# Performance work log

Measured on AMD Instinct MI355X. Metric: run time of the kernel, lower is better.

Reference implementation:

```python
import jax, jax.numpy as jnp
import numpy as np

D_MODEL = 2048
N_HEADS = 16
HEAD_DIM = D_MODEL // N_HEADS
D_FF = 4 * D_MODEL


def setup_inputs() -> dict:
    key = jax.random.key(0)
    ks = jax.random.split(key, 12)
    s = 1.0 / np.sqrt(D_MODEL)
    sf = 1.0 / np.sqrt(D_FF)
    return {
        "x": jax.random.normal(ks[0], (2, 2048, D_MODEL), dtype=jnp.float32),
        "wq": jax.random.uniform(ks[1], (D_MODEL, D_MODEL), jnp.float32, -s, s),
        "wk": jax.random.uniform(ks[2], (D_MODEL, D_MODEL), jnp.float32, -s, s),
        "wv": jax.random.uniform(ks[3], (D_MODEL, D_MODEL), jnp.float32, -s, s),
        "wo": jax.random.uniform(ks[4], (D_MODEL, D_MODEL), jnp.float32, -s, s),
        "w1": jax.random.uniform(ks[5], (D_MODEL, D_FF), jnp.float32, -s, s),
        "b1": jax.random.uniform(ks[6], (D_FF,), jnp.float32, -s, s),
        "w2": jax.random.uniform(ks[7], (D_FF, D_MODEL), jnp.float32, -sf, sf),
        "b2": jax.random.uniform(ks[8], (D_MODEL,), jnp.float32, -sf, sf),
        "g1": jnp.ones((D_MODEL,), jnp.float32),
        "be1": jnp.zeros((D_MODEL,), jnp.float32),
        "g2": jnp.ones((D_MODEL,), jnp.float32),
        "be2": jnp.zeros((D_MODEL,), jnp.float32),
    }


def _layernorm(x, g, b, eps=1e-5):
    mu = jnp.mean(x, axis=-1, keepdims=True)
    var = jnp.mean(jnp.square(x - mu), axis=-1, keepdims=True)
    return (x - mu) * jax.lax.rsqrt(var + eps) * g + b


def reference(x, wq, wk, wv, wo, w1, b1, w2, b2, g1, be1, g2, be2):
    B, S, D = x.shape
    residual = x
    h = _layernorm(x, g1, be1)
    # [B,S,D] -> [B,H,S,hd]
    q = (h @ wq).reshape(B, S, N_HEADS, HEAD_DIM).transpose(0, 2, 1, 3)
    k = (h @ wk).reshape(B, S, N_HEADS, HEAD_DIM).transpose(0, 2, 1, 3)
    v = (h @ wv).reshape(B, S, N_HEADS, HEAD_DIM).transpose(0, 2, 1, 3)
    scores = jnp.einsum("bhqd,bhkd->bhqk", q, k) / np.sqrt(HEAD_DIM).astype(np.float32)
    attn = jax.nn.softmax(scores, axis=-1)
    out = jnp.einsum("bhqk,bhkd->bhqd", attn, v)
    out = out.transpose(0, 2, 1, 3).reshape(B, S, D) @ wo
    x = residual + out
    residual = x
    h = _layernorm(x, g2, be2)
    h = jax.nn.gelu(h @ w1 + b1, approximate=False) @ w2 + b2
    return residual + h
```

## Files before the change

### kernel.cpp

```cpp
#include <hip/hip_runtime.h>
#include <cstdint>
#include <cstddef>

#define DM   2048
#define NH   16
#define HD   128
#define DFF  8192
#define SEQ  2048
#define NB   2
#define NTOK (NB * SEQ)

using bf16x8 = __attribute__((ext_vector_type(8))) __bf16;
using f32x4  = __attribute__((ext_vector_type(4))) float;

__device__ __forceinline__ unsigned short f2bf(float f) {
  unsigned int u = __float_as_uint(f);
  u += 0x7fffu + ((u >> 16) & 1u);
  return (unsigned short)(u >> 16);
}

__device__ __forceinline__ void gload16(const void* g, void* l) {
  __builtin_amdgcn_global_load_lds(
      (const __attribute__((address_space(1))) unsigned int*)g,
      (__attribute__((address_space(3))) unsigned int*)l, 16, 0, 0);
}

__device__ __forceinline__ f32x4 mfma16(bf16x8 a, bf16x8 b, f32x4 c) {
  return __builtin_amdgcn_mfma_f32_16x16x32_bf16(a, b, c, 0, 0, 0);
}

#define BARRIER() asm volatile("s_barrier" ::: "memory")
#define LGKM0()   asm volatile("s_waitcnt lgkmcnt(0)" ::: "memory")

__device__ __forceinline__ int xcd_swz(int hb, int nwg) {
  return (hb & 7) * (nwg >> 3) + (hb >> 3);
}

__device__ __forceinline__ void tc64_body(
    const float* __restrict__ src, unsigned short* __restrict__ dst,
    int R, int C, int r0, int c0) {
  __shared__ float tile[64][65];
  const int t = threadIdx.x;
#pragma unroll
  for (int j = 0; j < 4; ++j) {
    const int c = t + j * 256;
    const int row = c >> 4, col = (c & 15) * 4;
    float4 v = *(const float4*)(src + (size_t)(r0 + row) * C + c0 + col);
    tile[row][col] = v.x; tile[row][col + 1] = v.y;
    tile[row][col + 2] = v.z; tile[row][col + 3] = v.w;
  }
  __syncthreads();
#pragma unroll
  for (int j = 0; j < 4; ++j) {
    const int c = t + j * 256;
    const int drow = c >> 4, scol = (c & 15) * 4;
    union { unsigned short u[4]; ushort4 v; } pk;
    pk.u[0] = f2bf(tile[scol][drow]);
    pk.u[1] = f2bf(tile[scol + 1][drow]);
    pk.u[2] = f2bf(tile[scol + 2][drow]);
    pk.u[3] = f2bf(tile[scol + 3][drow]);
    *(ushort4*)(dst + (size_t)(c0 + drow) * R + r0 + scol) = pk.v;
  }
}

__global__ __launch_bounds__(256) void transpose_cast(
    const float* __restrict__ src, unsigned short* __restrict__ dst, int R, int C) {
  tc64_body(src, dst, R, C, blockIdx.y * 64, blockIdx.x * 64);
}

__global__ __launch_bounds__(256) void transpose_cast4(
    const float* __restrict__ wq, const float* __restrict__ wk,
    const float* __restrict__ wv, const float* __restrict__ wo,
    unsigned short* __restrict__ dqkv, unsigned short* __restrict__ dwo) {
  const int z = blockIdx.z;
  const float* src = (z == 0) ? wq : (z == 1) ? wk : (z == 2) ? wv : wo;
  unsigned short* dst = (z < 3) ? (dqkv + (size_t)z * 2048 * 2048) : dwo;
  tc64_body(src, dst, 2048, 2048, blockIdx.y * 64, blockIdx.x * 64);
}

__global__ __launch_bounds__(256) void ln_kernel(
    const float* __restrict__ x, const float* __restrict__ gam,
    const float* __restrict__ bet, unsigned short* __restrict__ out) {
  const int row = blockIdx.x, tid = threadIdx.x;
  const float* xr = x + (size_t)row * DM;
  float4 a = *(const float4*)(xr + tid * 8);
  float4 b = *(const float4*)(xr + tid * 8 + 4);
  float s  = a.x + a.y + a.z + a.w + b.x + b.y + b.z + b.w;
  float s2 = a.x*a.x + a.y*a.y + a.z*a.z + a.w*a.w +
             b.x*b.x + b.y*b.y + b.z*b.z + b.w*b.w;
#pragma unroll
  for (int off = 32; off > 0; off >>= 1) {
    s  += __shfl_xor(s, off);
    s2 += __shfl_xor(s2, off);
  }
  __shared__ float red[8];
  const int wid = tid >> 6;
  if ((tid & 63) == 0) { red[wid] = s; red[4 + wid] = s2; }
  __syncthreads();
  s  = red[0] + red[1] + red[2] + red[3];
  s2 = red[4] + red[5] + red[6] + red[7];
  const float mean = s * (1.0f / DM);
  const float var  = s2 * (1.0f / DM) - mean * mean;
  const float rstd = rsqrtf(var + 1e-5f);
  float4 g0 = *(const float4*)(gam + tid * 8);
  float4 g1 = *(const float4*)(gam + tid * 8 + 4);
  float4 e0 = *(const float4*)(bet + tid * 8);
  float4 e1 = *(const float4*)(bet + tid * 8 + 4);
  union { unsigned short u[8]; uint4 v; } pk;
  const float* av = (const float*)&a; const float* bv = (const float*)&b;
  const float* gv0 = (const float*)&g0; const float* gv1 = (const float*)&g1;
  const float* ev0 = (const float*)&e0; const float* ev1 = (const float*)&e1;
#pragma unroll
  for (int j = 0; j < 4; j++) pk.u[j]     = f2bf((av[j] - mean) * rstd * gv0[j] + ev0[j]);
#pragma unroll
  for (int j = 0; j < 4; j++) pk.u[4 + j] = f2bf((bv[j] - mean) * rstd * gv1[j] + ev1[j]);
  *(uint4*)(out + (size_t)row * DM + tid * 8) = pk.v;
}

template <int EPI>
__global__ __launch_bounds__(512, 2) void gemm256(
    const unsigned short* __restrict__ A, const unsigned short* __restrict__ Bt,
    int M, int N, int K,
    unsigned short* __restrict__ o0, unsigned short* __restrict__ o1,
    unsigned short* __restrict__ o2, float* __restrict__ fo,
    const float* __restrict__ e0, const float* __restrict__ e1) {
  __shared__ __attribute__((aligned(16))) unsigned short As[2][256 * 64];
  __shared__ __attribute__((aligned(16))) unsigned short Bs[2][256 * 64];
  const int tid = threadIdx.x;
  const int wid = tid >> 6, lane = tid & 63;
  const int wr = wid >> 2, wc = wid & 3;
  const int c16 = lane & 15, g = lane >> 4;
  const int m0 = blockIdx.y * 256, n0 = blockIdx.x * 256;

  const int c0 = tid, c1 = tid + 512;
  const int r0_ = c0 >> 3, s0_ = ((c0 & 7) ^ (r0_ & 7)) * 8;
  const int r1_ = c1 >> 3, s1_ = ((c1 & 7) ^ (r1_ & 7)) * 8;
  const unsigned short* a0p = A + (size_t)(m0 + r0_) * K + s0_;
  const unsigned short* a1p = A + (size_t)(m0 + r1_) * K + s1_;
  const unsigned short* b0p = Bt + (size_t)(n0 + r0_) * K + s0_;
  const unsigned short* b1p = Bt + (size_t)(n0 + r1_) * K + s1_;
  const size_t hstep = (size_t)128 * K;

  auto SA = [&](int buf, int h, int kt) {
    gload16(a0p + h * hstep + kt * 64, &As[buf][h * 8192 + c0 * 8]);
    gload16(a1p + h * hstep + kt * 64, &As[buf][h * 8192 + c1 * 8]);
  };
  auto SB = [&](int buf, int h, int kt) {
    gload16(b0p + h * hstep + kt * 64, &Bs[buf][h * 8192 + c0 * 8]);
    gload16(b1p + h * hstep + kt * 64, &Bs[buf][h * 8192 + c1 * 8]);
  };

  const int swz   = (c16 & 7) << 4;
  const int k0off = (g * 16) ^ swz;
  const int k1off = (64 + g * 16) ^ swz;

  f32x4 acc[8][4];
#pragma unroll
  for (int i = 0; i < 8; i++)
#pragma unroll
    for (int j = 0; j < 4; j++) acc[i][j] = f32x4{0.f, 0.f, 0.f, 0.f};

  bf16x8 af0[4][2], af1[4][2], bf0[2][2], bf1[2][2];

  const int NT = K >> 6;
  SA(0, 0, 0); SA(0, 1, 0); SB(0, 0, 0); SB(0, 1, 0);
  SB(1, 0, 1); SB(1, 1, 1); SA(1, 0, 1);
  asm volatile("s_waitcnt vmcnt(6)" ::: "memory");
  BARRIER();

  for (int t = 0; t < NT; ++t) {
    const int buf = t & 1;
    const char* Ac = (const char*)As[buf];
    const char* Bc = (const char*)Bs[buf];
    const bool st = (t + 2) < NT;
#pragma unroll
    for (int mi = 0; mi < 4; ++mi) {
      const int rb = (wr * 64 + mi * 16 + c16) * 128;
      af0[mi][0] = *(const bf16x8*)(Ac + rb + k0off);
      af0[mi][1] = *(const bf16x8*)(Ac + rb + k1off);
    }
#pragma unroll
    for (int ni = 0; ni < 2; ++ni) {
      const int rb0 = (wc * 32 + ni * 16 + c16) * 128;
      bf0[ni][0] = *(const bf16x8*)(Bc + rb0 + k0off);
      bf0[ni][1] = *(const bf16x8*)(Bc + rb0 + k1off);
      const int rb1 = (128 + wc * 32 + ni * 16 + c16) * 128;
      bf1[ni][0] = *(const bf16x8*)(Bc + rb1 + k0off);
      bf1[ni][1] = *(const bf16x8*)(Bc + rb1 + k1off);
    }
    if (t + 1 < NT) SA(buf ^ 1, 1, t + 1);
    BARRIER(); LGKM0();
    __builtin_amdgcn_s_setprio(1);
#pragma unroll
    for (int mi = 0; mi < 4; ++mi)
#pragma unroll
      for (int ni = 0; ni < 2; ++ni)
#pragma unroll
        for (int kk = 0; kk < 2; ++kk) {
          acc[mi][ni]     = mfma16(af0[mi][kk], bf0[ni][kk], acc[mi][ni]);
          acc[mi][2 + ni] = mfma16(af0[mi][kk], bf1[ni][kk], acc[mi][2 + ni]);
        }
    __builtin_amdgcn_s_setprio(0);
    BARRIER();
#pragma unroll
    for (int mi = 0; mi < 4; ++mi) {
      const int rb = (128 + wr * 64 + mi * 16 + c16) * 128;
      af1[mi][0] = *(const bf16x8*)(Ac + rb + k0off);
      af1[mi][1] = *(const bf16x8*)(Ac + rb + k1off);
    }
    if (st) { SB(buf, 0, t + 2); SB(buf, 1, t + 2); SA(buf, 0, t + 2); }
    BARRIER(); LGKM0();
    __builtin_amdgcn_s_setprio(1);
#pragma unroll
    for (int mi = 0; mi < 4; ++mi)
#pragma unroll
      for (int ni = 0; ni < 2; ++ni)
#pragma unroll
        for (int kk = 0; kk < 2; ++kk) {
          acc[4 + mi][2 + ni] = mfma16(af1[mi][kk], bf1[ni][kk], acc[4 + mi][2 + ni]);
          acc[4 + mi][ni]     = mfma16(af1[mi][kk], bf0[ni][kk], acc[4 + mi][ni]);
        }
    __builtin_amdgcn_s_setprio(0);
    if (st) { asm volatile("s_waitcnt vmcnt(6)" ::: "memory"); }
    else    { asm volatile("s_waitcnt vmcnt(0)" ::: "memory"); }
    BARRIER();
  }

#pragma unroll
  for (int mi = 0; mi < 8; ++mi) {
    const int arow = (mi < 4) ? (wr * 64 + mi * 16) : (128 + wr * 64 + (mi - 4) * 16);
#pragma unroll
    for (int ni = 0; ni < 4; ++ni) {
      const int bcol = (ni < 2) ? (wc * 32 + ni * 16) : (128 + wc * 32 + (ni - 2) * 16);
#pragma unroll
      for (int r = 0; r < 4; ++r) {
        const int row = m0 + arow + g * 4 + r;
        const int col = n0 + bcol + c16;
        const float v = acc[mi][ni][r];
        if constexpr (EPI == 2) {
          const float t2 = v + e0[col];
          const float ge = 0.5f * t2 * (1.0f + erff(t2 * 0.7071067811865476f));
          o0[(size_t)row * N + col] = f2bf(ge);
        } else {
          const size_t idx = (size_t)row * N + col;
          fo[idx] = (EPI == 1) ? (e0[idx] + v) : (e1[idx] + v + e0[col]);
        }
      }
    }
  }
}

template <int EPI>
__global__ __launch_bounds__(256, 2) void gemm128(
    const unsigned short* __restrict__ A, const unsigned short* __restrict__ Bt,
    int M, int N, int K,
    unsigned short* __restrict__ o0, unsigned short* __restrict__ o1,
    unsigned short* __restrict__ o2, float* __restrict__ fo,
    const float* __restrict__ e0, const float* __restrict__ e1) {
  __shared__ __attribute__((aligned(16))) unsigned short SM[4][128 * 64];
  const int tid = threadIdx.x;
  const int wid = tid >> 6, lane = tid & 63;
  const int m0 = blockIdx.y * 128, n0 = blockIdx.x * 128;
  const int wr = wid >> 1, wc = wid & 1;
  const int c16 = lane & 15, g = lane >> 4;

  const unsigned short *ap[4], *bp[4];
  int dsto[4];
#pragma unroll
  for (int j = 0; j < 4; ++j) {
    const int c = tid + j * 256;
    const int r = c >> 3, s = ((c & 7) ^ (r & 7)) * 8;
    ap[j] = A + (size_t)(m0 + r) * K + s;
    bp[j] = Bt + (size_t)(n0 + r) * K + s;
    dsto[j] = c * 8;
  }
  auto SA = [&](int buf, int kt) {
#pragma unroll
    for (int j = 0; j < 4; ++j) gload16(ap[j] + kt * 64, &SM[buf][dsto[j]]);
  };
  auto SB = [&](int buf, int kt) {
#pragma unroll
    for (int j = 0; j < 4; ++j) gload16(bp[j] + kt * 64, &SM[2 + buf][dsto[j]]);
  };

  const int swz   = (c16 & 7) << 4;
  const int k0off = (g * 16) ^ swz;
  const int k1off = (64 + g * 16) ^ swz;

  f32x4 acc[4][4];
#pragma unroll
  for (int i = 0; i < 4; i++)
#pragma unroll
    for (int j = 0; j < 4; j++) acc[i][j] = f32x4{0.f, 0.f, 0.f, 0.f};

  bf16x8 af[4][2], bfm[4][2];

  const int NT = K >> 6;
  SA(0, 0); SB(0, 0);
  __syncthreads();

  for (int t = 0; t < NT; ++t) {
    const int buf = t & 1;
    const char* Ac = (const char*)SM[buf];
    const char* Bc = (const char*)SM[2 + buf];
    if (t + 1 < NT) { SA(buf ^ 1, t + 1); SB(buf ^ 1, t + 1); }
#pragma unroll
    for (int mi = 0; mi < 4; ++mi) {
      const int rb = (wr * 64 + mi * 16 + c16) * 128;
      af[mi][0] = *(const bf16x8*)(Ac + rb + k0off);
      af[mi][1] = *(const bf16x8*)(Ac + rb + k1off);
    }
#pragma unroll
    for (int ni = 0; ni < 4; ++ni) {
      const int rb = (wc * 64 + ni * 16 + c16) * 128;
      bfm[ni][0] = *(const bf16x8*)(Bc + rb + k0off);
      bfm[ni][1] = *(const bf16x8*)(Bc + rb + k1off);
    }
    __builtin_amdgcn_s_setprio(1);
#pragma unroll
    for (int mi = 0; mi < 4; ++mi)
#pragma unroll
      for (int ni = 0; ni < 4; ++ni)
#pragma unroll
        for (int kk = 0; kk < 2; ++kk)
          acc[mi][ni] = mfma16(af[mi][kk], bfm[ni][kk], acc[mi][ni]);
    __builtin_amdgcn_s_setprio(0);
    __syncthreads();
  }

  if constexpr (EPI == 0) {
    const int which = n0 >> 11;
    if (which == 2) {
      unsigned short* Ls = &SM[0][0];
#pragma unroll
      for (int mi = 0; mi < 4; ++mi)
#pragma unroll
        for (int ni = 0; ni < 4; ++ni)
#pragma unroll
          for (int r = 0; r < 4; ++r) {
            const int s_loc = wr * 64 + mi * 16 + g * 4 + r;
            const int d_loc = wc * 64 + ni * 16 + c16;
            Ls[d_loc * 136 + s_loc] = f2bf(acc[mi][ni][r]);
          }
      __syncthreads();
      const int b  = m0 >> 11, s0v = m0 & 2047;
      const int hh = (n0 & 2047) >> 7;
      const size_t base = (size_t)(b * NH + hh) * HD * (size_t)SEQ;
#pragma unroll
      for (int it2 = 0; it2 < 2; ++it2) {
        const int hd = it2 * 64 + (tid >> 2);
        const int sc = (tid & 3) * 32;
#pragma unroll
        for (int j = 0; j < 4; ++j) {
          uint4 vv = *(const uint4*)&Ls[hd * 136 + sc + j * 8];
          *(uint4*)&o2[base + (size_t)hd * SEQ + s0v + sc + j * 8] = vv;
        }
      }
    } else {
#pragma unroll
      for (int mi = 0; mi < 4; ++mi)
#pragma unroll
        for (int ni = 0; ni < 4; ++ni)
#pragma unroll
          for (int r = 0; r < 4; ++r) {
            const int row = m0 + wr * 64 + mi * 16 + g * 4 + r;
            const int col = n0 + wc * 64 + ni * 16 + c16;
            const float v = acc[mi][ni][r];
            const int b = row >> 11, s = row & 2047;
            const int d = col & 2047;
            const int hh = d >> 7, hd = d & 127;
            const size_t bh = (size_t)(b * NH + hh);
            if (which == 0) o0[(bh * SEQ + s) * HD + hd] = f2bf(v * 0.127517434f);
            else            o1[(bh * SEQ + s) * HD + hd] = f2bf(v);
          }
    }
  } else {
#pragma unroll
    for (int mi = 0; mi < 4; ++mi) {
#pragma unroll
      for (int ni = 0; ni < 4; ++ni) {
#pragma unroll
        for (int r = 0; r < 4; ++r) {
          const int row = m0 + wr * 64 + mi * 16 + g * 4 + r;
          const int col = n0 + wc * 64 + ni * 16 + c16;
          const float v = acc[mi][ni][r];
          if constexpr (EPI == 2) {
            const float t2 = v + e0[col];
            const float ge = 0.5f * t2 * (1.0f + erff(t2 * 0.7071067811865476f));
            o0[(size_t)row * N + col] = f2bf(ge);
          } else {
            const size_t idx = (size_t)row * N + col;
            fo[idx] = (EPI == 1) ? (e0[idx] + v) : (e1[idx] + v + e0[col]);
          }
        }
      }
    }
  }
}

__global__ __launch_bounds__(256, 2) void attn_kernel(
    const unsigned short* __restrict__ q, const unsigned short* __restrict__ k,
    const unsigned short* __restrict__ vT, unsigned short* __restrict__ out) {
  __shared__ __attribute__((aligned(16))) unsigned short Ks[2][64 * 128];
  __shared__ __attribute__((aligned(16))) unsigned short Vs[2][128 * 64];
  __shared__ __attribute__((aligned(16))) unsigned short Ps[4 * 32 * 64];
  const int tid = threadIdx.x, wid = tid >> 6, lane = tid & 63;
  const int c16 = lane & 15, g = lane >> 4;
  const int vbk = xcd_swz(blockIdx.x, 512);
  const int qt = vbk & 15, h = (vbk >> 4) & 15, b = vbk >> 8;
  const int q0 = qt * 128;
  const unsigned short* qb = q + (size_t)(b * NH + h) * SEQ * HD;
  const unsigned short* kb = k + (size_t)(b * NH + h) * SEQ * HD;
  const unsigned short* vb = vT + (size_t)(b * NH + h) * HD * SEQ;

  bf16x8 aq[2][4];
#pragma unroll
  for (int mi = 0; mi < 2; mi++)
#pragma unroll
    for (int ks = 0; ks < 4; ks++)
      aq[mi][ks] = *(const bf16x8*)(qb + (size_t)(q0 + wid * 32 + mi * 16 + c16) * HD +
                                    ks * 32 + g * 8);

  f32x4 o[2][8] = {};
  float mrow[2][4], lrow[2][4];
#pragma unroll
  for (int mi = 0; mi < 2; mi++)
#pragma unroll
    for (int r = 0; r < 4; r++) { mrow[mi][r] = -1e30f; lrow[mi][r] = 0.f; }

  const int kRowB = tid >> 4;
  const int kChk  = (tid & 15) ^ (kRowB & 7);
  const int vRowB = tid >> 3;
  const int vChk  = (tid & 7) ^ (vRowB & 7);
  char* PsW = (char*)Ps + wid * 4096;

  auto STAGE = [&](int buf, int kv0) {
#pragma unroll
    for (int seg = 0; seg < 4; seg++) {
      gload16(kb + (size_t)(kv0 + seg * 16 + kRowB) * HD + kChk * 8,
              &Ks[buf][wid * 512 + seg * 2048]);
      gload16(vb + (size_t)(seg * 32 + vRowB) * SEQ + kv0 + vChk * 8,
              &Vs[buf][wid * 512 + seg * 2048]);
    }
  };

  STAGE(0, 0);
  __syncthreads();

  const int NIT = SEQ / 64;
  for (int it = 0; it < NIT; ++it) {
    const int cur = it & 1;
    if (it + 1 < NIT) STAGE(cur ^ 1, (it + 1) * 64);
    const char* Kc = (const char*)&Ks[cur][0];
    const char* Vc = (const char*)&Vs[cur][0];

    f32x4 sc[2][4] = {};
#pragma unroll
    for (int ks = 0; ks < 4; ks++) {
#pragma unroll
      for (int ni = 0; ni < 4; ni++) {
        const int kr = ni * 16 + c16;
        const int lin = kr * 256 + ks * 64 + g * 16;
        bf16x8 bk = *(const bf16x8*)(Kc + (lin ^ ((kr & 7) << 4)));
        sc[0][ni] = mfma16(aq[0][ks], bk, sc[0][ni]);
        sc[1][ni] = mfma16(aq[1][ks], bk, sc[1][ni]);
      }
    }

#pragma unroll
    for (int mi = 0; mi < 2; mi++) {
#pragma unroll
      for (int r = 0; r < 4; r++) {
        float pm = fmaxf(fmaxf(sc[mi][0][r], sc[mi][1][r]),
                         fmaxf(sc[mi][2][r], sc[mi][3][r]));
        pm = fmaxf(pm, __shfl_xor(pm, 1));
        pm = fmaxf(pm, __shfl_xor(pm, 2));
        pm = fmaxf(pm, __shfl_xor(pm, 4));
        pm = fmaxf(pm, __shfl_xor(pm, 8));
        if (!__all(pm <= mrow[mi][r])) {
          const float mnew = fmaxf(mrow[mi][r], pm);
          const float scal = exp2f(mrow[mi][r] - mnew);
          mrow[mi][r] = mnew;
          lrow[mi][r] *= scal;
#pragma unroll
          for (int nj = 0; nj < 8; nj++) o[mi][nj][r] *= scal;
        }
        float rs = 0.f;
        const int prow = mi * 16 + g * 4 + r;
#pragma unroll
        for (int ni = 0; ni < 4; ni++) {
          const float p = exp2f(sc[mi][ni][r] - mrow[mi][r]);
          rs += p;
          const int lin = prow * 128 + (ni * 16 + c16) * 2;
          *(unsigned short*)(PsW + (lin ^ ((prow & 7) << 4))) = f2bf(p);
        }
        lrow[mi][r] += rs;
      }
    }

#pragma unroll
    for (int ks2 = 0; ks2 < 2; ks2++) {
      bf16x8 pa[2];
#pragma unroll
      for (int mi = 0; mi < 2; mi++) {
        const int pr = mi * 16 + c16;
        const int lin = pr * 128 + ks2 * 64 + g * 16;
        pa[mi] = *(const bf16x8*)(PsW + (lin ^ ((pr & 7) << 4)));
      }
#pragma unroll
      for (int nj = 0; nj < 8; nj++) {
        const int vr = nj * 16 + c16;
        const int lin = vr * 128 + ks2 * 64 + g * 16;
        bf16x8 bv = *(const bf16x8*)(Vc + (lin ^ ((vr & 7) << 4)));
        o[0][nj] = mfma16(pa[0], bv, o[0][nj]);
        o[1][nj] = mfma16(pa[1], bv, o[1][nj]);
      }
    }
    __syncthreads();
  }

#pragma unroll
  for (int mi = 0; mi < 2; mi++)
#pragma unroll
    for (int r = 0; r < 4; r++) {
      float l = lrow[mi][r];
      l += __shfl_xor(l, 1);
      l += __shfl_xor(l, 2);
      l += __shfl_xor(l, 4);
      l += __shfl_xor(l, 8);
      const float inv = 1.0f / l;
      const int s = q0 + wid * 32 + mi * 16 + g * 4 + r;
#pragma unroll
      for (int nj = 0; nj < 8; nj++)
        out[((size_t)(b * SEQ + s)) * DM + h * HD + nj * 16 + c16] =
            f2bf(o[mi][nj][r] * inv);
    }
}

extern "C" void kernel_launch(void* const* d_in, const int* in_sizes, int n_in,
                              void* d_out, int out_size, void* d_ws, size_t ws_size,
                              hipStream_t stream) {
  const float* x  = (const float*)d_in[0];
  const float* wq = (const float*)d_in[1];
  const float* wk = (const float*)d_in[2];
  const float* wv = (const float*)d_in[3];
  const float* wo = (const float*)d_in[4];
  const float* w1 = (const float*)d_in[5];
  const float* b1 = (const float*)d_in[6];
  const float* w2 = (const float*)d_in[7];
  const float* b2 = (const float*)d_in[8];
  const float* g1 = (const float*)d_in[9];
  const float* be1 = (const float*)d_in[10];
  const float* g2 = (const float*)d_in[11];
  const float* be2 = (const float*)d_in[12];

  char* ws = (char*)d_ws;
  unsigned short* wqkvT = (unsigned short*)(ws + 0);
  unsigned short* woT   = (unsigned short*)(ws + 25165824);
  unsigned short* w1T   = (unsigned short*)(ws + 33554432);
  unsigned short* w2T   = (unsigned short*)(ws + 67108864);
  float*          x2    = (float*)(ws + 100663296);
  unsigned short* hbuf  = (unsigned short*)(ws + 134217728);
  unsigned short* qbuf  = (unsigned short*)(ws + 150994944);
  unsigned short* kbuf  = (unsigned short*)(ws + 167772160);
  unsigned short* vtbuf = (unsigned short*)(ws + 184549376);
  unsigned short* ffh   = (unsigned short*)(ws + 150994944);

  transpose_cast4<<<dim3(32, 32, 4), 256, 0, stream>>>(wq, wk, wv, wo, wqkvT, woT);
  transpose_cast<<<dim3(128, 32), 256, 0, stream>>>(w1, w1T, 2048, 8192);
  transpose_cast<<<dim3(32, 128), 256, 0, stream>>>(w2, w2T, 8192, 2048);

  ln_kernel<<<NTOK, 256, 0, stream>>>(x, g1, be1, hbuf);

  gemm128<0><<<dim3(48, 32), 256, 0, stream>>>(
      hbuf, wqkvT, NTOK, 6144, 2048, qbuf, kbuf, vtbuf, nullptr, nullptr, nullptr);

  attn_kernel<<<512, 256, 0, stream>>>(qbuf, kbuf, vtbuf, hbuf);

  gemm128<1><<<dim3(16, 32), 256, 0, stream>>>(
      hbuf, woT, NTOK, 2048, 2048, nullptr, nullptr, nullptr, x2, x, nullptr);

  ln_kernel<<<NTOK, 256, 0, stream>>>(x2, g2, be2, hbuf);

  gemm256<2><<<dim3(32, 16), 512, 0, stream>>>(
      hbuf, w1T, NTOK, DFF, 2048, ffh, nullptr, nullptr, nullptr, b1, nullptr);

  gemm128<3><<<dim3(16, 32), 256, 0, stream>>>(
      ffh, w2T, NTOK, 2048, DFF, nullptr, nullptr, nullptr, (float*)d_out, b2, x2);
}
```

Before: 633.2 us.

## Loop N-tiles inside gemm128 and replace gemm256 with multi-tile gemm128

Adds an NTN template parameter so each gemm128 workgroup handles several 128-wide N tiles in sequence, spaced 2048 columns apart. The grid is cut to 512 workgroups for the QKV GEMM (3 tiles each) and the FFN1 GEMM (4 tiles each). The 256x256 gemm256 kernel is removed, and FFN1 now runs on the smaller-tile kernel. The likely aim is to cut launch/tail imbalance with one persistent-like wave of workgroups. In exchange, the larger tile's data reuse is lost and parallelism within each block becomes serialized.

```diff
diff --git a/kernel.cpp b/kernel.cpp
--- a/kernel.cpp
+++ b/kernel.cpp
@@ -28,9 +28,6 @@
 __device__ __forceinline__ f32x4 mfma16(bf16x8 a, bf16x8 b, f32x4 c) {
   return __builtin_amdgcn_mfma_f32_16x16x32_bf16(a, b, c, 0, 0, 0);
 }
-
-#define BARRIER() asm volatile("s_barrier" ::: "memory")
-#define LGKM0()   asm volatile("s_waitcnt lgkmcnt(0)" ::: "memory")
 
 __device__ __forceinline__ int xcd_swz(int hb, int nwg) {
   return (hb & 7) * (nwg >> 3) + (hb >> 3);
@@ -117,140 +114,7 @@
   *(uint4*)(out + (size_t)row * DM + tid * 8) = pk.v;
 }
 
-template <int EPI>
-__global__ __launch_bounds__(512, 2) void gemm256(
-    const unsigned short* __restrict__ A, const unsigned short* __restrict__ Bt,
-    int M, int N, int K,
-    unsigned short* __restrict__ o0, unsigned short* __restrict__ o1,
-    unsigned short* __restrict__ o2, float* __restrict__ fo,
-    const float* __restrict__ e0, const float* __restrict__ e1) {
-  __shared__ __attribute__((aligned(16))) unsigned short As[2][256 * 64];
-  __shared__ __attribute__((aligned(16))) unsigned short Bs[2][256 * 64];
-  const int tid = threadIdx.x;
-  const int wid = tid >> 6, lane = tid & 63;
-  const int wr = wid >> 2, wc = wid & 3;
-  const int c16 = lane & 15, g = lane >> 4;
-  const int m0 = blockIdx.y * 256, n0 = blockIdx.x * 256;
-
-  const int c0 = tid, c1 = tid + 512;
-  const int r0_ = c0 >> 3, s0_ = ((c0 & 7) ^ (r0_ & 7)) * 8;
-  const int r1_ = c1 >> 3, s1_ = ((c1 & 7) ^ (r1_ & 7)) * 8;
-  const unsigned short* a0p = A + (size_t)(m0 + r0_) * K + s0_;
-  const unsigned short* a1p = A + (size_t)(m0 + r1_) * K + s1_;
-  const unsigned short* b0p = Bt + (size_t)(n0 + r0_) * K + s0_;
-  const unsigned short* b1p = Bt + (size_t)(n0 + r1_) * K + s1_;
-  const size_t hstep = (size_t)128 * K;
-
-  auto SA = [&](int buf, int h, int kt) {
-    gload16(a0p + h * hstep + kt * 64, &As[buf][h * 8192 + c0 * 8]);
-    gload16(a1p + h * hstep + kt * 64, &As[buf][h * 8192 + c1 * 8]);
-  };
-  auto SB = [&](int buf, int h, int kt) {
-    gload16(b0p + h * hstep + kt * 64, &Bs[buf][h * 8192 + c0 * 8]);
-    gload16(b1p + h * hstep + kt * 64, &Bs[buf][h * 8192 + c1 * 8]);
-  };
-
-  const int swz   = (c16 & 7) << 4;
-  const int k0off = (g * 16) ^ swz;
-  const int k1off = (64 + g * 16) ^ swz;
-
-  f32x4 acc[8][4];
-#pragma unroll
-  for (int i = 0; i < 8; i++)
-#pragma unroll
-    for (int j = 0; j < 4; j++) acc[i][j] = f32x4{0.f, 0.f, 0.f, 0.f};
-
-  bf16x8 af0[4][2], af1[4][2], bf0[2][2], bf1[2][2];
-
-  const int NT = K >> 6;
-  SA(0, 0, 0); SA(0, 1, 0); SB(0, 0, 0); SB(0, 1, 0);
-  SB(1, 0, 1); SB(1, 1, 1); SA(1, 0, 1);
-  asm volatile("s_waitcnt vmcnt(6)" ::: "memory");
-  BARRIER();
-
-  for (int t = 0; t < NT; ++t) {
-    const int buf = t & 1;
-    const char* Ac = (const char*)As[buf];
-    const char* Bc = (const char*)Bs[buf];
-    const bool st = (t + 2) < NT;
-#pragma unroll
-    for (int mi = 0; mi < 4; ++mi) {
-      const int rb = (wr * 64 + mi * 16 + c16) * 128;
-      af0[mi][0] = *(const bf16x8*)(Ac + rb + k0off);
-      af0[mi][1] = *(const bf16x8*)(Ac + rb + k1off);
-    }
-#pragma unroll
-    for (int ni = 0; ni < 2; ++ni) {
-      const int rb0 = (wc * 32 + ni * 16 + c16) * 128;
-      bf0[ni][0] = *(const bf16x8*)(Bc + rb0 + k0off);
-      bf0[ni][1] = *(const bf16x8*)(Bc + rb0 + k1off);
-      const int rb1 = (128 + wc * 32 + ni * 16 + c16) * 128;
-      bf1[ni][0] = *(const bf16x8*)(Bc + rb1 + k0off);
-      bf1[ni][1] = *(const bf16x8*)(Bc + rb1 + k1off);
-    }
-    if (t + 1 < NT) SA(buf ^ 1, 1, t + 1);
-    BARRIER(); LGKM0();
-    __builtin_amdgcn_s_setprio(1);
-#pragma unroll
-    for (int mi = 0; mi < 4; ++mi)
-#pragma unroll
-      for (int ni = 0; ni < 2; ++ni)
-#pragma unroll
-        for (int kk = 0; kk < 2; ++kk) {
-          acc[mi][ni]     = mfma16(af0[mi][kk], bf0[ni][kk], acc[mi][ni]);
-          acc[mi][2 + ni] = mfma16(af0[mi][kk], bf1[ni][kk], acc[mi][2 + ni]);
-        }
-    __builtin_amdgcn_s_setprio(0);
-    BARRIER();
-#pragma unroll
-    for (int mi = 0; mi < 4; ++mi) {
-      const int rb = (128 + wr * 64 + mi * 16 + c16) * 128;
-      af1[mi][0] = *(const bf16x8*)(Ac + rb + k0off);
-      af1[mi][1] = *(const bf16x8*)(Ac + rb + k1off);
-    }
-    if (st) { SB(buf, 0, t + 2); SB(buf, 1, t + 2); SA(buf, 0, t + 2); }
-    BARRIER(); LGKM0();
-    __builtin_amdgcn_s_setprio(1);
-#pragma unroll
-    for (int mi = 0; mi < 4; ++mi)
-#pragma unroll
-      for (int ni = 0; ni < 2; ++ni)
-#pragma unroll
-        for (int kk = 0; kk < 2; ++kk) {
-          acc[4 + mi][2 + ni] = mfma16(af1[mi][kk], bf1[ni][kk], acc[4 + mi][2 + ni]);
-          acc[4 + mi][ni]     = mfma16(af1[mi][kk], bf0[ni][kk], acc[4 + mi][ni]);
-        }
-    __builtin_amdgcn_s_setprio(0);
-    if (st) { asm volatile("s_waitcnt vmcnt(6)" ::: "memory"); }
-    else    { asm volatile("s_waitcnt vmcnt(0)" ::: "memory"); }
-    BARRIER();
-  }
-
-#pragma unroll
-  for (int mi = 0; mi < 8; ++mi) {
-    const int arow = (mi < 4) ? (wr * 64 + mi * 16) : (128 + wr * 64 + (mi - 4) * 16);
-#pragma unroll
-    for (int ni = 0; ni < 4; ++ni) {
-      const int bcol = (ni < 2) ? (wc * 32 + ni * 16) : (128 + wc * 32 + (ni - 2) * 16);
-#pragma unroll
-      for (int r = 0; r < 4; ++r) {
-        const int row = m0 + arow + g * 4 + r;
-        const int col = n0 + bcol + c16;
-        const float v = acc[mi][ni][r];
-        if constexpr (EPI == 2) {
-          const float t2 = v + e0[col];
-          const float ge = 0.5f * t2 * (1.0f + erff(t2 * 0.7071067811865476f));
-          o0[(size_t)row * N + col] = f2bf(ge);
-        } else {
-          const size_t idx = (size_t)row * N + col;
-          fo[idx] = (EPI == 1) ? (e0[idx] + v) : (e1[idx] + v + e0[col]);
-        }
-      }
-    }
-  }
-}
-
-template <int EPI>
+template <int EPI, int NTN>
 __global__ __launch_bounds__(256, 2) void gemm128(
     const unsigned short* __restrict__ A, const unsigned short* __restrict__ Bt,
     int M, int N, int K,
@@ -260,137 +124,147 @@
   __shared__ __attribute__((aligned(16))) unsigned short SM[4][128 * 64];
   const int tid = threadIdx.x;
   const int wid = tid >> 6, lane = tid & 63;
-  const int m0 = blockIdx.y * 128, n0 = blockIdx.x * 128;
+  const int m0 = blockIdx.y * 128;
+  const int n0b = blockIdx.x * 128;
   const int wr = wid >> 1, wc = wid & 1;
   const int c16 = lane & 15, g = lane >> 4;
 
-  const unsigned short *ap[4], *bp[4];
-  int dsto[4];
+  int srow[4], sslot[4], dsto[4];
 #pragma unroll
   for (int j = 0; j < 4; ++j) {
     const int c = tid + j * 256;
-    const int r = c >> 3, s = ((c & 7) ^ (r & 7)) * 8;
-    ap[j] = A + (size_t)(m0 + r) * K + s;
-    bp[j] = Bt + (size_t)(n0 + r) * K + s;
+    srow[j] = c >> 3; sslot[j] = ((c & 7) ^ ((c >> 3) & 7)) * 8;
     dsto[j] = c * 8;
   }
-  auto SA = [&](int buf, int kt) {
-#pragma unroll
-    for (int j = 0; j < 4; ++j) gload16(ap[j] + kt * 64, &SM[buf][dsto[j]]);
-  };
-  auto SB = [&](int buf, int kt) {
-#pragma unroll
-    for (int j = 0; j < 4; ++j) gload16(bp[j] + kt * 64, &SM[2 + buf][dsto[j]]);
-  };
+  const unsigned short* ap[4];
+#pragma unroll
+  for (int j = 0; j < 4; ++j) ap[j] = A + (size_t)(m0 + srow[j]) * K + sslot[j];
 
   const int swz   = (c16 & 7) << 4;
   const int k0off = (g * 16) ^ swz;
   const int k1off = (64 + g * 16) ^ swz;
-
-  f32x4 acc[4][4];
-#pragma unroll
-  for (int i = 0; i < 4; i++)
-#pragma unroll
-    for (int j = 0; j < 4; j++) acc[i][j] = f32x4{0.f, 0.f, 0.f, 0.f};
-
-  bf16x8 af[4][2], bfm[4][2];
-
   const int NT = K >> 6;
-  SA(0, 0); SB(0, 0);
-  __syncthreads();
-
-  for (int t = 0; t < NT; ++t) {
-    const int buf = t & 1;
-    const char* Ac = (const char*)SM[buf];
-    const char* Bc = (const char*)SM[2 + buf];
-    if (t + 1 < NT) { SA(buf ^ 1, t + 1); SB(buf ^ 1, t + 1); }
-#pragma unroll
-    for (int mi = 0; mi < 4; ++mi) {
-      const int rb = (wr * 64 + mi * 16 + c16) * 128;
-      af[mi][0] = *(const bf16x8*)(Ac + rb + k0off);
-      af[mi][1] = *(const bf16x8*)(Ac + rb + k1off);
-    }
-#pragma unroll
-    for (int ni = 0; ni < 4; ++ni) {
-      const int rb = (wc * 64 + ni * 16 + c16) * 128;
-      bfm[ni][0] = *(const bf16x8*)(Bc + rb + k0off);
-      bfm[ni][1] = *(const bf16x8*)(Bc + rb + k1off);
-    }
-    __builtin_amdgcn_s_setprio(1);
-#pragma unroll
-    for (int mi = 0; mi < 4; ++mi)
-#pragma unroll
-      for (int ni = 0; ni < 4; ++ni)
-#pragma unroll
-        for (int kk = 0; kk < 2; ++kk)
-          acc[mi][ni] = mfma16(af[mi][kk], bfm[ni][kk], acc[mi][ni]);
-    __builtin_amdgcn_s_setprio(0);
+
+#pragma unroll
+  for (int itn = 0; itn < NTN; ++itn) {
+    const int n0 = n0b + itn * 2048;
+    const unsigned short* bp[4];
+#pragma unroll
+    for (int j = 0; j < 4; ++j) bp[j] = Bt + (size_t)(n0 + srow[j]) * K + sslot[j];
+
+    auto SA = [&](int buf, int kt) {
+#pragma unroll
+      for (int j = 0; j < 4; ++j) gload16(ap[j] + kt * 64, &SM[buf][dsto[j]]);
+    };
+    auto SB = [&](int buf, int kt) {
+#pragma unroll
+      for (int j = 0; j < 4; ++j) gload16(bp[j] + kt * 64, &SM[2 + buf][dsto[j]]);
+    };
+
+    f32x4 acc[4][4];
+#pragma unroll
+    for (int i = 0; i < 4; i++)
+#pragma unroll
+      for (int j = 0; j < 4; j++) acc[i][j] = f32x4{0.f, 0.f, 0.f, 0.f};
+
+    bf16x8 af[4][2], bfm[4][2];
+
+    SA(0, 0); SB(0, 0);
     __syncthreads();
-  }
-
-  if constexpr (EPI == 0) {
-    const int which = n0 >> 11;
-    if (which == 2) {
-      unsigned short* Ls = &SM[0][0];
+
+    for (int t = 0; t < NT; ++t) {
+      const int buf = t & 1;
+      const char* Ac = (const char*)SM[buf];
+      const char* Bc = (const char*)SM[2 + buf];
+      if (t + 1 < NT) { SA(buf ^ 1, t + 1); SB(buf ^ 1, t + 1); }
+#pragma unroll
+      for (int mi = 0; mi < 4; ++mi) {
+        const int rb = (wr * 64 + mi * 16 + c16) * 128;
+        af[mi][0] = *(const bf16x8*)(Ac + rb + k0off);
+        af[mi][1] = *(const bf16x8*)(Ac + rb + k1off);
+      }
+#pragma unroll
+      for (int ni = 0; ni < 4; ++ni) {
+        const int rb = (wc * 64 + ni * 16 + c16) * 128;
+        bfm[ni][0] = *(const bf16x8*)(Bc + rb + k0off);
+        bfm[ni][1] = *(const bf16x8*)(Bc + rb + k1off);
+      }
+      __builtin_amdgcn_s_setprio(1);
 #pragma unroll
       for (int mi = 0; mi < 4; ++mi)
 #pragma unroll
         for (int ni = 0; ni < 4; ++ni)
 #pragma unroll
-          for (int r = 0; r < 4; ++r) {
-            const int s_loc = wr * 64 + mi * 16 + g * 4 + r;
-            const int d_loc = wc * 64 + ni * 16 + c16;
-            Ls[d_loc * 136 + s_loc] = f2bf(acc[mi][ni][r]);
+          for (int kk = 0; kk < 2; ++kk)
+            acc[mi][ni] = mfma16(af[mi][kk], bfm[ni][kk], acc[mi][ni]);
+      __builtin_amdgcn_s_setprio(0);
+      __syncthreads();
+    }
+
+    if constexpr (EPI == 0) {
+      const int which = n0 >> 11;
+      if (which == 2) {
+        unsigned short* Ls = &SM[0][0];
+#pragma unroll
+        for (int mi = 0; mi < 4; ++mi)
+#pragma unroll
+          for (int ni = 0; ni < 4; ++ni)
+#pragma unroll
+            for (int r = 0; r < 4; ++r) {
+              const int s_loc = wr * 64 + mi * 16 + g * 4 + r;
+              const int d_loc = wc * 64 + ni * 16 + c16;
+              Ls[d_loc * 136 + s_loc] = f2bf(acc[mi][ni][r]);
+            }
+        __syncthreads();
+        const int b  = m0 >> 11, s0v = m0 & 2047;
+        const int hh = (n0 & 2047) >> 7;
+        const size_t base = (size_t)(b * NH + hh) * HD * (size_t)SEQ;
+#pragma unroll
+        for (int it2 = 0; it2 < 2; ++it2) {
+          const int hd = it2 * 64 + (tid >> 2);
+          const int sc = (tid & 3) * 32;
+#pragma unroll
+          for (int j = 0; j < 4; ++j) {
+            uint4 vv = *(const uint4*)&Ls[hd * 136 + sc + j * 8];
+            *(uint4*)&o2[base + (size_t)hd * SEQ + s0v + sc + j * 8] = vv;
           }
-      __syncthreads();
-      const int b  = m0 >> 11, s0v = m0 & 2047;
-      const int hh = (n0 & 2047) >> 7;
-      const size_t base = (size_t)(b * NH + hh) * HD * (size_t)SEQ;
-#pragma unroll
-      for (int it2 = 0; it2 < 2; ++it2) {
-        const int hd = it2 * 64 + (tid >> 2);
-        const int sc = (tid & 3) * 32;
-#pragma unroll
-        for (int j = 0; j < 4; ++j) {
-          uint4 vv = *(const uint4*)&Ls[hd * 136 + sc + j * 8];
-          *(uint4*)&o2[base + (size_t)hd * SEQ + s0v + sc + j * 8] = vv;
         }
+      } else {
+#pragma unroll
+        for (int mi = 0; mi < 4; ++mi)
+#pragma unroll
+          for (int ni = 0; ni < 4; ++ni)
+#pragma unroll
+            for (int r = 0; r < 4; ++r) {
+              const int row = m0 + wr * 64 + mi * 16 + g * 4 + r;
+              const int col = n0 + wc * 64 + ni * 16 + c16;
+              const float v = acc[mi][ni][r];
+              const int b = row >> 11, s = row & 2047;
+              const int d = col & 2047;
+              const int hh = d >> 7, hd = d & 127;
+              const size_t bh = (size_t)(b * NH + hh);
+              if (which == 0) o0[(bh * SEQ + s) * HD + hd] = f2bf(v * 0.127517434f);
+              else            o1[(bh * SEQ + s) * HD + hd] = f2bf(v);
+            }
       }
     } else {
 #pragma unroll
-      for (int mi = 0; mi < 4; ++mi)
-#pragma unroll
-        for (int ni = 0; ni < 4; ++ni)
+      for (int mi = 0; mi < 4; ++mi) {
+#pragma unroll
+        for (int ni = 0; ni < 4; ++ni) {
 #pragma unroll
           for (int r = 0; r < 4; ++r) {
             const int row = m0 + wr * 64 + mi * 16 + g * 4 + r;
             const int col = n0 + wc * 64 + ni * 16 + c16;
             const float v = acc[mi][ni][r];
-            const int b = row >> 11, s = row & 2047;
-            const int d = col & 2047;
-            const int hh = d >> 7, hd = d & 127;
-            const size_t bh = (size_t)(b * NH + hh);
-            if (which == 0) o0[(bh * SEQ + s) * HD + hd] = f2bf(v * 0.127517434f);
-            else            o1[(bh * SEQ + s) * HD + hd] = f2bf(v);
-          }
-    }
-  } else {
-#pragma unroll
-    for (int mi = 0; mi < 4; ++mi) {
-#pragma unroll
-      for (int ni = 0; ni < 4; ++ni) {
-#pragma unroll
-        for (int r = 0; r < 4; ++r) {
-          const int row = m0 + wr * 64 + mi * 16 + g * 4 + r;
-          const int col = n0 + wc * 64 + ni * 16 + c16;
-          const float v = acc[mi][ni][r];
-          if constexpr (EPI == 2) {
-            const float t2 = v + e0[col];
-            const float ge = 0.5f * t2 * (1.0f + erff(t2 * 0.7071067811865476f));
-            o0[(size_t)row * N + col] = f2bf(ge);
-          } else {
-            const size_t idx = (size_t)row * N + col;
-            fo[idx] = (EPI == 1) ? (e0[idx] + v) : (e1[idx] + v + e0[col]);
+            if constexpr (EPI == 2) {
+              const float t2 = v + e0[col];
+              const float ge = 0.5f * t2 * (1.0f + erff(t2 * 0.7071067811865476f));
+              o0[(size_t)row * N + col] = f2bf(ge);
+            } else {
+              const size_t idx = (size_t)row * N + col;
+              fo[idx] = (EPI == 1) ? (e0[idx] + v) : (e1[idx] + v + e0[col]);
+            }
           }
         }
       }
@@ -572,19 +446,19 @@
 
   ln_kernel<<<NTOK, 256, 0, stream>>>(x, g1, be1, hbuf);
 
-  gemm128<0><<<dim3(48, 32), 256, 0, stream>>>(
+  gemm128<0, 3><<<dim3(16, 32), 256, 0, stream>>>(
       hbuf, wqkvT, NTOK, 6144, 2048, qbuf, kbuf, vtbuf, nullptr, nullptr, nullptr);
 
   attn_kernel<<<512, 256, 0, stream>>>(qbuf, kbuf, vtbuf, hbuf);
 
-  gemm128<1><<<dim3(16, 32), 256, 0, stream>>>(
+  gemm128<1, 1><<<dim3(16, 32), 256, 0, stream>>>(
       hbuf, woT, NTOK, 2048, 2048, nullptr, nullptr, nullptr, x2, x, nullptr);
 
   ln_kernel<<<NTOK, 256, 0, stream>>>(x2, g2, be2, hbuf);
 
-  gemm256<2><<<dim3(32, 16), 512, 0, stream>>>(
+  gemm128<2, 4><<<dim3(16, 32), 256, 0, stream>>>(
       hbuf, w1T, NTOK, DFF, 2048, ffh, nullptr, nullptr, nullptr, b1, nullptr);
 
-  gemm128<3><<<dim3(16, 32), 256, 0, stream>>>(
+  gemm128<3, 1><<<dim3(16, 32), 256, 0, stream>>>(
       ffh, w2T, NTOK, 2048, DFF, nullptr, nullptr, nullptr, (float*)d_out, b2, x2);
 }
```

New measurement: 689.0 us. 1.09x slower.
